# Kernel optimization log

Measured on AMD Instinct MI355X. Metric: run time of the kernel, lower is better.

Reference implementation:

```python
import jax, jax.numpy as jnp
import numpy as np

D_MODEL = 1024
N_HEADS = 16
D_K = D_MODEL // N_HEADS
ROPE_BASE = 500000.0
RMS_EPS = 1e-10


def _rms_norm(x, w):
    # RMSNorm over last dim (per-head d_k): w * x / sqrt(mean(x^2) + eps)
    rms = jnp.sqrt(jnp.mean(x * x, axis=-1, keepdims=True) + RMS_EPS)
    return w * (x / rms)


def _rotate_half(x):
    x1, x2 = x[..., : x.shape[-1] // 2], x[..., x.shape[-1] // 2:]
    return jnp.concatenate([-x2, x1], axis=-1)


def _rope_cos_sin(seq_len):
    inv_freq = 1.0 / (ROPE_BASE ** (jnp.arange(0, D_K, 2, dtype=jnp.float32) / D_K))
    t = jnp.arange(seq_len, dtype=jnp.float32)
    freqs = jnp.outer(t, inv_freq)                # (S, d_k/2)
    emb = jnp.concatenate([freqs, freqs], axis=-1)  # (S, d_k)
    return jnp.cos(emb), jnp.sin(emb)


def setup_inputs() -> dict:
    key = jax.random.key(0)
    ks = jax.random.split(key, 9)
    B, S, D = 2, 2048, D_MODEL
    scale = 1.0 / np.sqrt(D)
    return {
        "q": jax.random.normal(ks[0], (B, S, D), jnp.float32),
        "k": jax.random.normal(ks[1], (B, S, D), jnp.float32),
        "v": jax.random.normal(ks[2], (B, S, D), jnp.float32),
        "w_q": jax.random.normal(ks[3], (D, D), jnp.float32) * scale,
        "w_k": jax.random.normal(ks[4], (D, D), jnp.float32) * scale,
        "w_v": jax.random.normal(ks[5], (D, D), jnp.float32) * scale,
        "w_o": jax.random.normal(ks[6], (D, D), jnp.float32) * scale,
        "q_norm_w": jnp.ones((D_K,), jnp.float32),
        "k_norm_w": jnp.ones((D_K,), jnp.float32),
    }


def reference(q, k, v, w_q, w_k, w_v, w_o, q_norm_w, k_norm_w):
    B, S, D = q.shape
    H, Dk = N_HEADS, D_K

    # QKV projections (nn.Linear without bias: x @ W.T), split into heads
    query = jnp.einsum("bsd,ed->bse", q, w_q).reshape(B, S, H, Dk).transpose(0, 2, 1, 3)
    key_ = jnp.einsum("bsd,ed->bse", k, w_k).reshape(B, S, H, Dk).transpose(0, 2, 1, 3)
    value = jnp.einsum("bsd,ed->bse", v, w_v).reshape(B, S, H, Dk).transpose(0, 2, 1, 3)

    # QK-norm (per-head RMSNorm)
    query = _rms_norm(query, q_norm_w)
    key_ = _rms_norm(key_, k_norm_w)

    # RoPE, default positions 0..S-1
    cos, sin = _rope_cos_sin(S)          # (S, d_k)
    cos = cos[None, None]                # (1,1,S,d_k)
    sin = sin[None, None]
    query = query * cos + _rotate_half(query) * sin
    key_ = key_ * cos + _rotate_half(key_) * sin

    # Causal scaled dot-product attention
    scale = 1.0 / jnp.sqrt(jnp.asarray(Dk, query.dtype))
    scores = jnp.einsum("bhqd,bhkd->bhqk", query, key_) * scale
    causal = jnp.tril(jnp.ones((S, S), dtype=bool))
    scores = jnp.where(causal, scores, jnp.finfo(scores.dtype).min)
    attn = jax.nn.softmax(scores, axis=-1)
    out = jnp.einsum("bhqk,bhkd->bhqd", attn, value)  # (B,H,S,d_k)

    out = out.transpose(0, 2, 1, 3).reshape(B, S, D)
    return jnp.einsum("bsd,ed->bse", out, w_o)
```

## Files before the change

### kernel.cpp

```cpp
#include <hip/hip_runtime.h>
#include <cstdint>
#include <cstddef>

typedef __bf16 bf16;
typedef __bf16 bf16x4_t __attribute__((ext_vector_type(4)));
typedef __bf16 bf16x8_t __attribute__((ext_vector_type(8)));
typedef float  f32x4_t  __attribute__((ext_vector_type(4)));

#define GLD_LDS16(g, l)                                                              \
  __builtin_amdgcn_global_load_lds((const __attribute__((address_space(1))) void*)(g), \
                                   (__attribute__((address_space(3))) void*)(l), 16, 0, 0)

#define S_WAITCNT_VMCNT(N) asm volatile("s_waitcnt vmcnt(" #N ")" ::: "memory")
#define S_BARRIER() asm volatile("s_barrier" ::: "memory")

__global__ __launch_bounds__(256) void cvt_kernel(
    const float* __restrict__ q, const float* __restrict__ k, const float* __restrict__ v,
    const float* __restrict__ wq, const float* __restrict__ wk, const float* __restrict__ wv,
    const float* __restrict__ wo,
    bf16* __restrict__ qb, bf16* __restrict__ kb, bf16* __restrict__ vb,
    bf16* __restrict__ wqb, bf16* __restrict__ wkb, bf16* __restrict__ wvb,
    bf16* __restrict__ wob)
{
  const float* src; bf16* dst; int n;
  switch (blockIdx.y) {
    case 0: src = q;  dst = qb;  n = 4194304; break;
    case 1: src = k;  dst = kb;  n = 4194304; break;
    case 2: src = v;  dst = vb;  n = 4194304; break;
    case 3: src = wq; dst = wqb; n = 1048576; break;
    case 4: src = wk; dst = wkb; n = 1048576; break;
    case 5: src = wv; dst = wvb; n = 1048576; break;
    default: src = wo; dst = wob; n = 1048576; break;
  }
  const int i = (blockIdx.x * 256 + threadIdx.x) * 4;
  if (i >= n) return;
  const float4 f = *(const float4*)(src + i);
  bf16x4_t o;
  o[0] = (bf16)f.x; o[1] = (bf16)f.y; o[2] = (bf16)f.z; o[3] = (bf16)f.w;
  *(bf16x4_t*)(dst + i) = o;
}

__device__ __forceinline__ void gemm_core(const bf16* __restrict__ A,
                                          const bf16* __restrict__ W,
                                          int m0, int n0, bf16* smem,
                                          f32x4_t (&acc)[4][4])
{
  const int K = 1024;
  bf16* As = smem;
  bf16* Bs = smem + 12288;
  const int t = threadIdx.x;
  const int lane = t & 63, w = t >> 6;
  const int l16 = lane & 15, qd = lane >> 4;
  const int wm = (w & 1) * 64, wn = (w >> 1) * 64;

  const int p8 = t >> 3;
  const int vslot = (t & 7) ^ (p8 & 7);
  const int srow = 2 * p8 + (vslot >> 2);
  const int scc = vslot & 3;
  const bf16* ag0 = A + (size_t)(m0 + srow) * K + scc * 8;
  const bf16* ag1 = A + (size_t)(m0 + 64 + srow) * K + scc * 8;
  const bf16* wg0 = W + (size_t)(n0 + srow) * K + scc * 8;
  const bf16* wg1 = W + (size_t)(n0 + 64 + srow) * K + scc * 8;
  const int lo0 = (w * 64) * 8;
  const int lo1 = (256 + w * 64) * 8;

  const int rslot = (((l16 & 1) * 4 + qd) ^ ((l16 >> 1) & 7)) * 8;
  const int abase = (wm >> 6) * 2048 + (l16 >> 1) * 64 + rslot;
  const int bbase = (wn >> 6) * 2048 + (l16 >> 1) * 64 + rslot;

#define STAGEG(k0_, b_)                                  \
  do {                                                   \
    GLD_LDS16(ag0 + (k0_), &As[(b_) * 4096 + lo0]);      \
    GLD_LDS16(ag1 + (k0_), &As[(b_) * 4096 + lo1]);      \
    GLD_LDS16(wg0 + (k0_), &Bs[(b_) * 4096 + lo0]);      \
    GLD_LDS16(wg1 + (k0_), &Bs[(b_) * 4096 + lo1]);      \
  } while (0)

  STAGEG(0, 0);
  STAGEG(32, 1);

  for (int k0 = 0; k0 < K; k0 += 32) {
    const int it = k0 >> 5;
    const int cb = it - (it / 3) * 3;
    if (k0 + 32 < K) S_WAITCNT_VMCNT(4); else S_WAITCNT_VMCNT(0);
    S_BARRIER();
    if (k0 + 64 < K) {
      const int nb = (it + 2) - ((it + 2) / 3) * 3;
      STAGEG(k0 + 64, nb);
    }
    bf16x8_t af[4], bfg[4];
#pragma unroll
    for (int i = 0; i < 4; ++i)
      af[i] = *(const bf16x8_t*)(&As[cb * 4096 + abase + i * 512]);
#pragma unroll
    for (int j = 0; j < 4; ++j)
      bfg[j] = *(const bf16x8_t*)(&Bs[cb * 4096 + bbase + j * 512]);
#pragma unroll
    for (int i = 0; i < 4; ++i)
#pragma unroll
      for (int j = 0; j < 4; ++j)
        acc[i][j] = __builtin_amdgcn_mfma_f32_16x16x32_bf16(af[i], bfg[j], acc[i][j], 0, 0, 0);
  }
#undef STAGEG
}

__global__ __launch_bounds__(256) void gemm_qkv(
    const bf16* __restrict__ qb, const bf16* __restrict__ wqb,
    const bf16* __restrict__ kb, const bf16* __restrict__ wkb,
    const bf16* __restrict__ vb, const bf16* __restrict__ wvb,
    const float* __restrict__ qnw, const float* __restrict__ knw,
    bf16* __restrict__ Qp, bf16* __restrict__ Kp, bf16* __restrict__ Vt)
{
  __shared__ bf16 smem[24576];
  const int z = blockIdx.z;
  const bf16 *A, *W;
  if (z == 0)      { A = qb; W = wqb; }
  else if (z == 1) { A = kb; W = wkb; }
  else             { A = vb; W = wvb; }

  const int m0 = blockIdx.y * 128, n0 = blockIdx.x * 128;
  f32x4_t acc[4][4] = {};
  gemm_core(A, W, m0, n0, smem, acc);

  const int t = threadIdx.x;
  const int lane = t & 63, w = t >> 6;
  const int l16 = lane & 15, qd = lane >> 4;
  const int wm = (w & 1) * 64;
  const int h = blockIdx.x * 2 + (w >> 1);
  const int b = m0 >> 11;

  if (z == 2) {
#pragma unroll
    for (int i = 0; i < 4; ++i) {
      const int sq = (m0 & 2047) + wm + i * 16 + qd * 4;
      const int pos = (sq & ~31) + 8 * qd + 4 * (i & 1);
#pragma unroll
      for (int j = 0; j < 4; ++j) {
        const int dk = j * 16 + l16;
        bf16x4_t ov;
#pragma unroll
        for (int r = 0; r < 4; ++r) ov[r] = (bf16)acc[i][j][r];
        *(bf16x4_t*)(Vt + ((size_t)((b * 16 + h) * 64 + dk)) * 2048 + pos) = ov;
      }
    }
    return;
  }

  const float* nw = (z == 0) ? qnw : knw;
  const float osc = (z == 0) ? 0.125f * 1.44269504088896f : 1.0f;
  bf16* Out = (z == 0) ? Qp : Kp;

  float nwv[4];
#pragma unroll
  for (int j = 0; j < 4; ++j) nwv[j] = nw[j * 16 + l16];
  float invf[2];
#pragma unroll
  for (int jj = 0; jj < 2; ++jj) {
    const int d = jj * 16 + l16;
    invf[jj] = __builtin_amdgcn_exp2f(-(float)(2 * d) * (18.93156857f / 64.0f)) * 0.15915494309f;
  }

  __syncthreads();
  bf16* ep = smem + w * 1152;

#pragma unroll
  for (int i = 0; i < 4; ++i) {
    const int sbase = (m0 & 2047) + wm + i * 16 + qd * 4;
    float ssq[4];
#pragma unroll
    for (int r = 0; r < 4; ++r) {
      ssq[r] = 0.f;
#pragma unroll
      for (int j = 0; j < 4; ++j) ssq[r] += acc[i][j][r] * acc[i][j][r];
    }
#pragma unroll
    for (int off = 1; off < 16; off <<= 1)
#pragma unroll
      for (int r = 0; r < 4; ++r) ssq[r] += __shfl_xor(ssq[r], off);

    float xn[4][4];
#pragma unroll
    for (int r = 0; r < 4; ++r) {
      const float inv = 1.0f / sqrtf(ssq[r] * (1.0f / 64.0f) + 1e-10f);
#pragma unroll
      for (int j = 0; j < 4; ++j) xn[j][r] = acc[i][j][r] * inv * nwv[j];
    }
#pragma unroll
    for (int jj = 0; jj < 2; ++jj) {
#pragma unroll
      for (int r = 0; r < 4; ++r) {
        const int s = sbase + r;
        float rev = (float)s * invf[jj];
        rev = rev - floorf(rev);
        const float cv = __builtin_amdgcn_cosf(rev);
        const float sv = __builtin_amdgcn_sinf(rev);
        const float o1 = (xn[jj][r] * cv - xn[jj + 2][r] * sv) * osc;
        const float o2 = (xn[jj + 2][r] * cv + xn[jj][r] * sv) * osc;
        const int prow = qd * 4 + r;
        ep[prow * 72 + jj * 16 + l16] = (bf16)o1;
        ep[prow * 72 + 32 + jj * 16 + l16] = (bf16)o2;
      }
    }
    const int sg = (m0 & 2047) + wm + i * 16 + l16;
    const bf16x8_t t0 = *(const bf16x8_t*)(ep + l16 * 72 + qd * 16);
    const bf16x8_t t1 = *(const bf16x8_t*)(ep + l16 * 72 + qd * 16 + 8);
    bf16* gb = Out + ((size_t)(b * 16 + h) * 2048 + sg) * 64 + qd * 16;
    *(bf16x8_t*)(gb) = t0;
    *(bf16x8_t*)(gb + 8) = t1;
  }
}

__global__ __launch_bounds__(256) void gemm_out_k(
    const bf16* __restrict__ Ob, const bf16* __restrict__ wob, float* __restrict__ out)
{
  __shared__ bf16 smem[24576];
  const int N = 1024;

  const int orig = blockIdx.x + 8 * blockIdx.y;
  const int wgid = (orig & 7) * 32 + (orig >> 3);
  const int by = wgid >> 3, bx = wgid & 7;

  const int m0 = by * 128, n0 = bx * 128;
  f32x4_t acc[4][4] = {};
  gemm_core(Ob, wob, m0, n0, smem, acc);

  const int t = threadIdx.x;
  const int lane = t & 63, w = t >> 6;
  const int l16 = lane & 15, qd = lane >> 4;
  const int wm = (w & 1) * 64, wn = (w >> 1) * 64;

  __syncthreads();
  float* epf = (float*)smem + w * 1088;

#pragma unroll
  for (int i = 0; i < 4; ++i) {
#pragma unroll
    for (int j = 0; j < 4; ++j)
#pragma unroll
      for (int r = 0; r < 4; ++r)
        epf[(qd * 4 + r) * 68 + j * 16 + l16] = acc[i][j][r];
    const int row = m0 + wm + i * 16 + l16;
#pragma unroll
    for (int c = 0; c < 4; ++c) {
      const f32x4_t vv = *(const f32x4_t*)(epf + l16 * 68 + qd * 16 + c * 4);
      *(f32x4_t*)(out + (size_t)row * N + n0 + wn + qd * 16 + c * 4) = vv;
    }
  }
}

__global__ __launch_bounds__(512) void flash_attn(
    const bf16* __restrict__ Qp, const bf16* __restrict__ Kp,
    const bf16* __restrict__ Vt, bf16* __restrict__ O)
{
  const int S = 2048;

  const int orig = blockIdx.x + 16 * blockIdx.y;
  const int wgid = (orig & 7) * 64 + (orig >> 3);
  const int bx = wgid & 15, bh = wgid >> 4;

  const int qt = 15 - bx;
  const int t = threadIdx.x;
  const int lane = t & 63, w = t >> 6;
  const int l16 = lane & 15, qd = lane >> 4;

  __shared__ bf16 Ks[3][64 * 64];
  __shared__ bf16 Vs[3][64 * 64];

  const int qrow = qt * 128 + w * 16 + l16;
  const bf16* qbase = Qp + ((size_t)bh * S + qrow) * 64 + qd * 8;
  const bf16x8_t qf0 = *(const bf16x8_t*)qbase;
  const bf16x8_t qf1 = *(const bf16x8_t*)(qbase + 32);

  f32x4_t o_acc[4] = {};
  float l_i = 0.f;

  const int srow = t >> 3;
  const int scol = ((t & 7) ^ (srow & 7)) * 8;
  const bf16* kg = Kp + ((size_t)bh * S + srow) * 64 + scol;
  const bf16* vg = Vt + ((size_t)(bh * 64 + srow)) * S + scol;
  const int lo = w * 512;

  const int sw = l16 & 7;

#define STAGE(kt_, b_)                                 \
  do {                                                 \
    GLD_LDS16(kg + (size_t)(kt_) * 4096, &Ks[b_][lo]); \
    GLD_LDS16(vg + (kt_) * 64, &Vs[b_][lo]);           \
  } while (0)

  const int ktmax = 2 * qt + 1;
  STAGE(0, 0);
  STAGE(1, 1);

  for (int kt = 0; kt <= ktmax; ++kt) {
    const int cb = kt - (kt / 3) * 3;
    if (kt < ktmax) S_WAITCNT_VMCNT(2); else S_WAITCNT_VMCNT(0);
    S_BARRIER();
    if (kt + 2 <= ktmax) {
      const int nb = (kt + 2) - ((kt + 2) / 3) * 3;
      STAGE(kt + 2, nb);
    }

    if (kt == ktmax && w < 4) continue;

    f32x4_t sf[4];
    __builtin_amdgcn_s_setprio(1);
#pragma unroll
    for (int nt = 0; nt < 4; ++nt) {
      sf[nt][0] = -12.f; sf[nt][1] = -12.f; sf[nt][2] = -12.f; sf[nt][3] = -12.f;
      const bf16x8_t kf0 = *(const bf16x8_t*)(&Ks[cb][(nt * 16 + l16) * 64 + ((0 + qd) ^ sw) * 8]);
      const bf16x8_t kf1 = *(const bf16x8_t*)(&Ks[cb][(nt * 16 + l16) * 64 + ((4 + qd) ^ sw) * 8]);
      sf[nt] = __builtin_amdgcn_mfma_f32_16x16x32_bf16(kf0, qf0, sf[nt], 0, 0, 0);
      sf[nt] = __builtin_amdgcn_mfma_f32_16x16x32_bf16(kf1, qf1, sf[nt], 0, 0, 0);
    }
    __builtin_amdgcn_s_setprio(0);

    if (kt >= ktmax - 1) {
      const int kofs = (kt - 2 * qt) * 64;
      const int q_local = w * 16 + l16;
#pragma unroll
      for (int nt = 0; nt < 4; ++nt)
#pragma unroll
        for (int r = 0; r < 4; ++r)
          if (kofs + nt * 16 + qd * 4 + r > q_local) sf[nt][r] = -100.f;
    }

    bf16x4_t pb[4];
#pragma unroll
    for (int nt = 0; nt < 4; ++nt)
#pragma unroll
      for (int r = 0; r < 4; ++r) {
        const float p = __builtin_amdgcn_exp2f(sf[nt][r]);
        l_i += p;
        pb[nt][r] = (bf16)p;
      }

    __builtin_amdgcn_s_setprio(1);
#pragma unroll
    for (int nt2 = 0; nt2 < 2; ++nt2) {
      bf16x8_t pf;
#pragma unroll
      for (int r = 0; r < 4; ++r) { pf[r] = pb[2 * nt2][r]; pf[4 + r] = pb[2 * nt2 + 1][r]; }
#pragma unroll
      for (int dt = 0; dt < 4; ++dt) {
        const int row = dt * 16 + l16;
        const bf16x8_t vf =
            *(const bf16x8_t*)(&Vs[cb][row * 64 + ((4 * nt2 + qd) ^ sw) * 8]);
        o_acc[dt] = __builtin_amdgcn_mfma_f32_16x16x32_bf16(vf, pf, o_acc[dt], 0, 0, 0);
      }
    }
    __builtin_amdgcn_s_setprio(0);
  }
#undef STAGE

  l_i += __shfl_xor(l_i, 16);
  l_i += __shfl_xor(l_i, 32);

  const int b = bh >> 4, h = bh & 15;
  const float inv_l = 1.0f / l_i;
  const int qg = qt * 128 + w * 16 + l16;
#pragma unroll
  for (int dt = 0; dt < 4; ++dt) {
    bf16x4_t ov;
#pragma unroll
    for (int r = 0; r < 4; ++r) ov[r] = (bf16)(o_acc[dt][r] * inv_l);
    *(bf16x4_t*)(O + ((size_t)(b * S + qg)) * 1024 + h * 64 + dt * 16 + qd * 4) = ov;
  }
}

extern "C" void kernel_launch(void* const* d_in, const int* in_sizes, int n_in,
                              void* d_out, int out_size, void* d_ws, size_t ws_size,
                              hipStream_t stream)
{
  const float* q   = (const float*)d_in[0];
  const float* k   = (const float*)d_in[1];
  const float* v   = (const float*)d_in[2];
  const float* wq  = (const float*)d_in[3];
  const float* wk  = (const float*)d_in[4];
  const float* wv  = (const float*)d_in[5];
  const float* wo  = (const float*)d_in[6];
  const float* qnw = (const float*)d_in[7];
  const float* knw = (const float*)d_in[8];

  char* ws = (char*)d_ws;
  const size_t MB = 1u << 20;
  bf16* qb  = (bf16*)(ws + 0 * MB);
  bf16* kb  = (bf16*)(ws + 8 * MB);
  bf16* vb  = (bf16*)(ws + 16 * MB);
  bf16* wqb = (bf16*)(ws + 24 * MB);
  bf16* wkb = (bf16*)(ws + 26 * MB);
  bf16* wvb = (bf16*)(ws + 28 * MB);
  bf16* wob = (bf16*)(ws + 30 * MB);
  bf16* Qp  = (bf16*)(ws + 32 * MB);
  bf16* Kp  = (bf16*)(ws + 40 * MB);
  bf16* Vtr = (bf16*)(ws + 48 * MB);
  bf16* Oattn = qb;

  cvt_kernel<<<dim3(4096, 7), 256, 0, stream>>>(q, k, v, wq, wk, wv, wo,
                                                qb, kb, vb, wqb, wkb, wvb, wob);
  gemm_qkv<<<dim3(8, 32, 3), 256, 0, stream>>>(qb, wqb, kb, wkb, vb, wvb,
                                               qnw, knw, Qp, Kp, Vtr);
  flash_attn<<<dim3(16, 32), 512, 0, stream>>>(Qp, Kp, Vtr, Oattn);
  gemm_out_k<<<dim3(8, 32), 256, 0, stream>>>(Oattn, wob, (float*)d_out);
}
```

Before: 211.3 us.

## Enlarge QKV projection tiles to 256x256 with 512-thread blocks

The QKV projection GEMM now uses 256x256 output tiles per workgroup with 8 waves, each computing a 128x64 sub-tile, instead of 128x128 tiles with 4 waves. The gemm_core call is replaced by an inlined triple-buffered global-to-LDS pipeline with doubled shared memory. The aim is more operand reuse per LDS load and less global traffic per FLOP. In exchange the grid drops from 768 to 192 workgroups, which may underfill the GPU's compute units, and register pressure rises with a 32-accumulator-tile state per wave.

Result: no change. 212.5 us (+0.6%).

```diff
diff --git a/kernel.cpp b/kernel.cpp
--- a/kernel.cpp
+++ b/kernel.cpp
@@ -104,35 +104,88 @@
 #undef STAGEG
 }
 
-__global__ __launch_bounds__(256) void gemm_qkv(
+__global__ __launch_bounds__(512) void gemm_qkv(
     const bf16* __restrict__ qb, const bf16* __restrict__ wqb,
     const bf16* __restrict__ kb, const bf16* __restrict__ wkb,
     const bf16* __restrict__ vb, const bf16* __restrict__ wvb,
     const float* __restrict__ qnw, const float* __restrict__ knw,
     bf16* __restrict__ Qp, bf16* __restrict__ Kp, bf16* __restrict__ Vt)
 {
-  __shared__ bf16 smem[24576];
+  __shared__ bf16 smem[49152];
+  const int K = 1024;
   const int z = blockIdx.z;
   const bf16 *A, *W;
   if (z == 0)      { A = qb; W = wqb; }
   else if (z == 1) { A = kb; W = wkb; }
   else             { A = vb; W = wvb; }
 
-  const int m0 = blockIdx.y * 128, n0 = blockIdx.x * 128;
-  f32x4_t acc[4][4] = {};
-  gemm_core(A, W, m0, n0, smem, acc);
-
+  const int m0 = blockIdx.y * 256, n0 = blockIdx.x * 256;
   const int t = threadIdx.x;
   const int lane = t & 63, w = t >> 6;
   const int l16 = lane & 15, qd = lane >> 4;
-  const int wm = (w & 1) * 64;
-  const int h = blockIdx.x * 2 + (w >> 1);
-  const int b = m0 >> 11;
+  const int wm = (w >> 2) * 128, wn = (w & 3) * 64;
+
+  bf16* As = smem;
+  bf16* Bs = smem + 24576;
+
+  const int p8 = t >> 3;
+  const int vslot = (t & 7) ^ (p8 & 7);
+  const int srow = 2 * p8 + (vslot >> 2);
+  const int scc = vslot & 3;
+  const bf16* ag0 = A + (size_t)(m0 + srow) * K + scc * 8;
+  const bf16* ag1 = A + (size_t)(m0 + 128 + srow) * K + scc * 8;
+  const bf16* wg0 = W + (size_t)(n0 + srow) * K + scc * 8;
+  const bf16* wg1 = W + (size_t)(n0 + 128 + srow) * K + scc * 8;
+  const int lo0 = t * 8;
+  const int lo1 = 4096 + t * 8;
+
+  const int rslot = (((l16 & 1) * 4 + qd) ^ ((l16 >> 1) & 7)) * 8;
+  const int abase = (w >> 2) * 4096 + (l16 >> 1) * 64 + rslot;
+  const int bbase = ((w >> 1) & 1) * 4096 + ((w & 1) * 32 + (l16 >> 1)) * 64 + rslot;
+
+  f32x4_t acc[8][4] = {};
+
+#define STAGEG(k0_, b_)                                  \
+  do {                                                   \
+    GLD_LDS16(ag0 + (k0_), &As[(b_) * 8192 + lo0]);      \
+    GLD_LDS16(ag1 + (k0_), &As[(b_) * 8192 + lo1]);      \
+    GLD_LDS16(wg0 + (k0_), &Bs[(b_) * 8192 + lo0]);      \
+    GLD_LDS16(wg1 + (k0_), &Bs[(b_) * 8192 + lo1]);      \
+  } while (0)
+
+  STAGEG(0, 0);
+  STAGEG(32, 1);
+
+  for (int kk = 0; kk < 32; ++kk) {
+    const int cb = kk - (kk / 3) * 3;
+    if (kk < 31) S_WAITCNT_VMCNT(4); else S_WAITCNT_VMCNT(0);
+    S_BARRIER();
+    if (kk + 2 < 32) {
+      const int nb = (kk + 2) - ((kk + 2) / 3) * 3;
+      STAGEG((kk + 2) * 32, nb);
+    }
+    bf16x8_t af[8], bfg[4];
+#pragma unroll
+    for (int i = 0; i < 8; ++i)
+      af[i] = *(const bf16x8_t*)(&As[cb * 8192 + abase + i * 512]);
+#pragma unroll
+    for (int j = 0; j < 4; ++j)
+      bfg[j] = *(const bf16x8_t*)(&Bs[cb * 8192 + bbase + j * 512]);
+#pragma unroll
+    for (int i = 0; i < 8; ++i)
+#pragma unroll
+      for (int j = 0; j < 4; ++j)
+        acc[i][j] = __builtin_amdgcn_mfma_f32_16x16x32_bf16(af[i], bfg[j], acc[i][j], 0, 0, 0);
+  }
+#undef STAGEG
+
+  const int h = blockIdx.x * 4 + (w & 3);
+  const int b = (m0 + wm) >> 11;
 
   if (z == 2) {
 #pragma unroll
-    for (int i = 0; i < 4; ++i) {
-      const int sq = (m0 & 2047) + wm + i * 16 + qd * 4;
+    for (int i = 0; i < 8; ++i) {
+      const int sq = ((m0 + wm) & 2047) + i * 16 + qd * 4;
       const int pos = (sq & ~31) + 8 * qd + 4 * (i & 1);
 #pragma unroll
       for (int j = 0; j < 4; ++j) {
@@ -164,8 +217,8 @@
   bf16* ep = smem + w * 1152;
 
 #pragma unroll
-  for (int i = 0; i < 4; ++i) {
-    const int sbase = (m0 & 2047) + wm + i * 16 + qd * 4;
+  for (int i = 0; i < 8; ++i) {
+    const int sbase = ((m0 + wm) & 2047) + i * 16 + qd * 4;
     float ssq[4];
 #pragma unroll
     for (int r = 0; r < 4; ++r) {
@@ -201,7 +254,7 @@
         ep[prow * 72 + 32 + jj * 16 + l16] = (bf16)o2;
       }
     }
-    const int sg = (m0 & 2047) + wm + i * 16 + l16;
+    const int sg = ((m0 + wm) & 2047) + i * 16 + l16;
     const bf16x8_t t0 = *(const bf16x8_t*)(ep + l16 * 72 + qd * 16);
     const bf16x8_t t1 = *(const bf16x8_t*)(ep + l16 * 72 + qd * 16 + 8);
     bf16* gb = Out + ((size_t)(b * 16 + h) * 2048 + sg) * 64 + qd * 16;
@@ -398,7 +451,7 @@
 
   cvt_kernel<<<dim3(4096, 7), 256, 0, stream>>>(q, k, v, wq, wk, wv, wo,
                                                 qb, kb, vb, wqb, wkb, wvb, wob);
-  gemm_qkv<<<dim3(8, 32, 3), 256, 0, stream>>>(qb, wqb, kb, wkb, vb, wvb,
+  gemm_qkv<<<dim3(4, 16, 3), 512, 0, stream>>>(qb, wqb, kb, wkb, vb, wvb,
                                                qnw, knw, Qp, Kp, Vtr);
   flash_attn<<<dim3(16, 32), 512, 0, stream>>>(Qp, Kp, Vtr, Oattn);
   gemm_out_k<<<dim3(8, 32), 256, 0, stream>>>(Oattn, wob, (float*)d_out);
```
